# Optimization experiments

Hardware: AMD Instinct MI355X
Metric: run time of the kernel (lower is better)

The kernel has to match this reference:

```python
import jax, jax.numpy as jnp
import numpy as np


def setup_inputs() -> dict:
    key = jax.random.key(0)
    k1, k2, k3 = jax.random.split(key, 3)
    B, F, D = 8192, 4096, 1024
    x = jax.random.normal(k1, (B, D), dtype=jnp.float32)
    mu = jax.random.normal(k2, (F, D), dtype=jnp.float32)
    # keep scales strictly positive and well-conditioned
    scale_diag = jax.random.uniform(k3, (F, D), dtype=jnp.float32, minval=0.5, maxval=1.5)
    return {"x": x, "mu": mu, "scale_diag": scale_diag}


def reference(x, mu, scale_diag):
    # Unnormalized diag-Gaussian log prob for every (batch, feature) pair:
    #   out[b, f] = sum_d -0.5 * ((x[b,d] - mu[f,d]) / scale[f,d])^2
    # Expanded to GEMM form (quadratic expansion):
    #   -0.5 * ( x^2 @ inv2.T  -  2 * x @ (mu*inv2).T  +  sum_d mu^2*inv2 )
    inv2 = 1.0 / (scale_diag * scale_diag)            # [F, D]
    xx = jnp.matmul(x * x, inv2.T)                    # [B, F]
    xm = jnp.matmul(x, (mu * inv2).T)                 # [B, F]
    mm = jnp.sum(mu * mu * inv2, axis=-1)             # [F]
    return -0.5 * (xx - 2.0 * xm + mm[None, :])       # [B, F]
```

## Files before the change

### kernel.cpp

```cpp
#include <hip/hip_runtime.h>
#include <hip/hip_bf16.h>
#include <cstdint>

#define B_SZ 8192
#define F_SZ 4096
#define D_SZ 1024
#define K_SZ 2048

typedef __bf16 bf16x8 __attribute__((ext_vector_type(8)));
typedef float f32x4 __attribute__((ext_vector_type(4)));
typedef float fvec4 __attribute__((ext_vector_type(4)));
typedef unsigned short u16x4 __attribute__((ext_vector_type(4)));

__device__ __forceinline__ unsigned short f2bf(float f) {
    union { float f; unsigned u; } c; c.f = f;
    unsigned r = c.u + 0x7fff + ((c.u >> 16) & 1);
    return (unsigned short)(r >> 16);
}

__device__ __forceinline__ void async16(const void* g, void* l) {
    __builtin_amdgcn_global_load_lds(
        (__attribute__((address_space(1))) void*)g,
        (__attribute__((address_space(3))) void*)l, 16, 0, 0);
}

__global__ __launch_bounds__(256) void prep(const float* __restrict__ x,
                                            const float* __restrict__ mu,
                                            const float* __restrict__ sd,
                                            unsigned short* __restrict__ A,
                                            unsigned short* __restrict__ W,
                                            float* __restrict__ nmm) {
    const int tid = threadIdx.x;
    if (blockIdx.x < 4096) {
        const size_t o0 = (size_t)blockIdx.x * 2048 + tid * 4;
        fvec4 v0 = *(const fvec4*)(x + o0);
        fvec4 v1 = *(const fvec4*)(x + o0 + 1024);
        #pragma unroll
        for (int h = 0; h < 2; ++h) {
            fvec4 v = h ? v1 : v0;
            size_t oo = o0 + h * 1024;
            size_t b = oo >> 10;
            int d = (int)(oo & 1023);
            u16x4 xx, xs;
            xx.x = f2bf(v.x * v.x); xx.y = f2bf(v.y * v.y);
            xx.z = f2bf(v.z * v.z); xx.w = f2bf(v.w * v.w);
            xs.x = f2bf(v.x); xs.y = f2bf(v.y);
            xs.z = f2bf(v.z); xs.w = f2bf(v.w);
            *(u16x4*)(A + b * K_SZ + d) = xx;
            *(u16x4*)(A + b * K_SZ + 1024 + d) = xs;
        }
    } else {
        const int f = blockIdx.x - 4096;
        const int d = tid * 4;
        size_t off = (size_t)f * D_SZ + d;
        fvec4 m = *(const fvec4*)(mu + off);
        fvec4 s = *(const fvec4*)(sd + off);
        float i0 = 1.0f / (s.x * s.x), i1 = 1.0f / (s.y * s.y);
        float i2 = 1.0f / (s.z * s.z), i3 = 1.0f / (s.w * s.w);
        u16x4 wi, wm;
        wi.x = f2bf(i0); wi.y = f2bf(i1); wi.z = f2bf(i2); wi.w = f2bf(i3);
        wm.x = f2bf(-2.0f * m.x * i0); wm.y = f2bf(-2.0f * m.y * i1);
        wm.z = f2bf(-2.0f * m.z * i2); wm.w = f2bf(-2.0f * m.w * i3);
        size_t wb = (size_t)f * K_SZ + d;
        *(u16x4*)(W + wb) = wi;
        *(u16x4*)(W + wb + 1024) = wm;
        float mm = m.x * m.x * i0 + m.y * m.y * i1 + m.z * m.z * i2 + m.w * m.w * i3;
        #pragma unroll
        for (int o = 32; o > 0; o >>= 1) mm += __shfl_down(mm, o, 64);
        __shared__ float red[4];
        if ((tid & 63) == 0) red[tid >> 6] = mm;
        __syncthreads();
        if (tid == 0) nmm[f] = -0.5f * (red[0] + red[1] + red[2] + red[3]);
    }
}

__global__ __launch_bounds__(256) void gemm_bt(const unsigned short* __restrict__ A,
                                               const unsigned short* __restrict__ W,
                                               const float* __restrict__ nmm,
                                               float* __restrict__ out) {
    __shared__ __align__(16) unsigned short sA[128 * 32];
    __shared__ __align__(16) unsigned short sB[128 * 32];

    const int tid  = threadIdx.x;
    const int wave = tid >> 6;
    const int lane = tid & 63;
    const int wm = (wave >> 1) * 64;
    const int wn = (wave & 1) * 64;
    const int tileM = blockIdx.y * 128;
    const int tileN = blockIdx.x * 128;
    const int r16  = lane & 15;
    const int quad = lane >> 4;

    const int row0 = tid >> 2;
    const int col0 = (tid & 3) * 8;
    unsigned short* ldsA0 = sA + (wave * 64) * 8;
    unsigned short* ldsA1 = sA + (256 + wave * 64) * 8;
    unsigned short* ldsB0 = sB + (wave * 64) * 8;
    unsigned short* ldsB1 = sB + (256 + wave * 64) * 8;

    const f32x4 vzero = {0.f, 0.f, 0.f, 0.f};
    f32x4 acc[4][4];
    #pragma unroll
    for (int i = 0; i < 4; ++i)
        #pragma unroll
        for (int j = 0; j < 4; ++j) acc[i][j] = vzero;

    for (int k0 = 0; k0 < K_SZ; k0 += 32) {
        async16(A + (size_t)(tileM + row0) * K_SZ + k0 + col0, ldsA0);
        async16(A + (size_t)(tileM + row0 + 64) * K_SZ + k0 + col0, ldsA1);
        async16(W + (size_t)(tileN + row0) * K_SZ + k0 + col0, ldsB0);
        async16(W + (size_t)(tileN + row0 + 64) * K_SZ + k0 + col0, ldsB1);
        __syncthreads();

        bf16x8 af[4], bfr[4];
        #pragma unroll
        for (int i = 0; i < 4; ++i)
            af[i] = *(const bf16x8*)(sA + (wm + i * 16 + r16) * 32 + quad * 8);
        #pragma unroll
        for (int j = 0; j < 4; ++j)
            bfr[j] = *(const bf16x8*)(sB + (wn + j * 16 + r16) * 32 + quad * 8);
        #pragma unroll
        for (int i = 0; i < 4; ++i)
            #pragma unroll
            for (int j = 0; j < 4; ++j)
                acc[i][j] = __builtin_amdgcn_mfma_f32_16x16x32_bf16(
                    af[i], bfr[j], acc[i][j], 0, 0, 0);
        __syncthreads();
    }

    int   fc[4];
    float cj[4];
    #pragma unroll
    for (int j = 0; j < 4; ++j) {
        fc[j] = tileN + wn + j * 16 + r16;
        cj[j] = nmm[fc[j]];
    }
    #pragma unroll
    for (int i = 0; i < 4; ++i) {
        int mbase = tileM + wm + i * 16 + quad * 4;
        #pragma unroll
        for (int r = 0; r < 4; ++r) {
            float* orow = out + (size_t)(mbase + r) * F_SZ;
            #pragma unroll
            for (int j = 0; j < 4; ++j)
                orow[fc[j]] = -0.5f * acc[i][j][r] + cj[j];
        }
    }
}

extern "C" void kernel_launch(void* const* d_in, const int* in_sizes, int n_in,
                              void* d_out, int out_size, void* d_ws, size_t ws_size,
                              hipStream_t stream) {
    const float* x  = (const float*)d_in[0];
    const float* mu = (const float*)d_in[1];
    const float* sd = (const float*)d_in[2];
    float* out = (float*)d_out;

    unsigned short* A = (unsigned short*)d_ws;
    unsigned short* W = A + (size_t)B_SZ * K_SZ;
    float* nmm = (float*)(W + (size_t)F_SZ * K_SZ);

    prep<<<8192, 256, 0, stream>>>(x, mu, sd, A, W, nmm);
    gemm_bt<<<dim3(F_SZ / 128, B_SZ / 128), 256, 0, stream>>>(A, W, nmm, out);
}
```

Baseline: 332.2 us.

## Rewrite GEMM as 256x256 tile, 8-wave, double-buffered pipeline with swizzled LDS

The bf16 GEMM moves from 128x128 tiles with 4 waves and a single LDS buffer to 256x256 tiles with 8 waves. It double-buffers K=64 slabs and issues async global-to-LDS loads for the next stage between phases, using explicit vmcnt and lgkmcnt waits, raw barriers and setprio around the MFMA blocks. An XOR swizzle on LDS columns is meant to avoid bank conflicts. The goal is to hide global load latency behind MFMA work and raise arithmetic intensity per tile. The cost is 128KB of LDS, higher register pressure, and hand-tuned wait counts that may be fragile.

```diff
diff --git a/kernel.cpp b/kernel.cpp
--- a/kernel.cpp
+++ b/kernel.cpp
@@ -74,70 +74,123 @@
     }
 }
 
-__global__ __launch_bounds__(256) void gemm_bt(const unsigned short* __restrict__ A,
-                                               const unsigned short* __restrict__ W,
-                                               const float* __restrict__ nmm,
-                                               float* __restrict__ out) {
-    __shared__ __align__(16) unsigned short sA[128 * 32];
-    __shared__ __align__(16) unsigned short sB[128 * 32];
+__global__ __launch_bounds__(512, 2) void gemm_bt(const unsigned short* __restrict__ A,
+                                                  const unsigned short* __restrict__ W,
+                                                  const float* __restrict__ nmm,
+                                                  float* __restrict__ out) {
+    __shared__ __align__(16) unsigned short sA[2][2][256 * 32];
+    __shared__ __align__(16) unsigned short sB[2][2][256 * 32];
 
     const int tid  = threadIdx.x;
     const int wave = tid >> 6;
     const int lane = tid & 63;
-    const int wm = (wave >> 1) * 64;
-    const int wn = (wave & 1) * 64;
-    const int tileM = blockIdx.y * 128;
-    const int tileN = blockIdx.x * 128;
     const int r16  = lane & 15;
     const int quad = lane >> 4;
-
-    const int row0 = tid >> 2;
-    const int col0 = (tid & 3) * 8;
-    unsigned short* ldsA0 = sA + (wave * 64) * 8;
-    unsigned short* ldsA1 = sA + (256 + wave * 64) * 8;
-    unsigned short* ldsB0 = sB + (wave * 64) * 8;
-    unsigned short* ldsB1 = sB + (256 + wave * 64) * 8;
+    const int wmB  = (wave >> 2) * 128;
+    const int wnB  = (wave & 3) * 64;
+    const int tileM = blockIdx.y * 256;
+    const int tileN = blockIdx.x * 256;
+
+    const int srow   = tid >> 2;
+    const int schunk = tid & 3;
 
     const f32x4 vzero = {0.f, 0.f, 0.f, 0.f};
-    f32x4 acc[4][4];
+    f32x4 acc[8][4];
     #pragma unroll
-    for (int i = 0; i < 4; ++i)
+    for (int i = 0; i < 8; ++i)
         #pragma unroll
         for (int j = 0; j < 4; ++j) acc[i][j] = vzero;
 
-    for (int k0 = 0; k0 < K_SZ; k0 += 32) {
-        async16(A + (size_t)(tileM + row0) * K_SZ + k0 + col0, ldsA0);
-        async16(A + (size_t)(tileM + row0 + 64) * K_SZ + k0 + col0, ldsA1);
-        async16(W + (size_t)(tileN + row0) * K_SZ + k0 + col0, ldsB0);
-        async16(W + (size_t)(tileN + row0 + 64) * K_SZ + k0 + col0, ldsB1);
-        __syncthreads();
-
-        bf16x8 af[4], bfr[4];
-        #pragma unroll
-        for (int i = 0; i < 4; ++i)
-            af[i] = *(const bf16x8*)(sA + (wm + i * 16 + r16) * 32 + quad * 8);
-        #pragma unroll
-        for (int j = 0; j < 4; ++j)
-            bfr[j] = *(const bf16x8*)(sB + (wn + j * 16 + r16) * 32 + quad * 8);
-        #pragma unroll
-        for (int i = 0; i < 4; ++i)
-            #pragma unroll
-            for (int j = 0; j < 4; ++j)
-                acc[i][j] = __builtin_amdgcn_mfma_f32_16x16x32_bf16(
-                    af[i], bfr[j], acc[i][j], 0, 0, 0);
-        __syncthreads();
-    }
+    bf16x8 af[4], bfr[4];
+
+#define BARW() __builtin_amdgcn_s_barrier()
+#define LGK()  asm volatile("s_waitcnt lgkmcnt(0)" ::: "memory")
+#define VM4()  asm volatile("s_waitcnt vmcnt(4)" ::: "memory")
+#define VM0()  asm volatile("s_waitcnt vmcnt(0)" ::: "memory")
+
+#define STAGE(S, G, TB, DB, KK, KT)                                          \
+    { _Pragma("unroll")                                                      \
+      for (int is_ = 0; is_ < 2; ++is_) {                                    \
+          int rr_ = is_ * 128 + srow;                                        \
+          int gc_ = ((schunk ^ (rr_ & 3)) << 3);                             \
+          async16(G + (size_t)((TB) + rr_) * K_SZ + (KT) * 64 + (KK) * 32 + gc_, \
+                  &S[DB][KK][0] + is_ * 4096 + wave * 512);                  \
+      } }
+
+#define READ_A(I0, DB, KK)                                                   \
+    { _Pragma("unroll")                                                      \
+      for (int i_ = 0; i_ < 4; ++i_) {                                       \
+          int row_ = wmB + ((I0) + i_) * 16 + r16;                           \
+          af[i_] = *(const bf16x8*)(&sA[DB][KK][0] + row_ * 32 +             \
+                                    (((quad ^ row_) & 3) << 3));             \
+      } }
+
+#define READ_B(DB, KK)                                                       \
+    { _Pragma("unroll")                                                      \
+      for (int j_ = 0; j_ < 4; ++j_) {                                       \
+          int row_ = wnB + j_ * 16 + r16;                                    \
+          bfr[j_] = *(const bf16x8*)(&sB[DB][KK][0] + row_ * 32 +            \
+                                     (((quad ^ row_) & 3) << 3));            \
+      } }
+
+#define MFMA16(I0)                                                           \
+    __builtin_amdgcn_s_setprio(1);                                          \
+    { _Pragma("unroll")                                                      \
+      for (int i_ = 0; i_ < 4; ++i_)                                         \
+          _Pragma("unroll")                                                  \
+          for (int j_ = 0; j_ < 4; ++j_)                                     \
+              acc[(I0) + i_][j_] = __builtin_amdgcn_mfma_f32_16x16x32_bf16(  \
+                  af[i_], bfr[j_], acc[(I0) + i_][j_], 0, 0, 0); }           \
+    __builtin_amdgcn_s_setprio(0);
+
+#define PH(RB, I0, DB, KK, DOSTG, SBUF, G, TB, SDB, SKK, SKT, VM)            \
+    { if (RB) READ_B(DB, KK)                                                 \
+      READ_A(I0, DB, KK)                                                     \
+      if (DOSTG) STAGE(SBUF, G, TB, SDB, SKK, SKT)                           \
+      BARW(); LGK();                                                         \
+      MFMA16(I0)                                                             \
+      if ((VM) == 4) VM4(); else if ((VM) == 0) VM0();                       \
+      BARW(); }
+
+#define ITER(T, S58)                                                         \
+    PH(1, 0, 0, 0, 1,      sA, A, tileM, 1, 0, (T) + 1, -1)                  \
+    PH(0, 4, 0, 0, 1,      sB, W, tileN, 1, 0, (T) + 1, 4)                   \
+    PH(1, 0, 0, 1, 1,      sA, A, tileM, 1, 1, (T) + 1, -1)                  \
+    PH(0, 4, 0, 1, 1,      sB, W, tileN, 1, 1, (T) + 1, 4)                   \
+    PH(1, 0, 1, 0, (S58),  sA, A, tileM, 0, 0, (T) + 2, -1)                  \
+    PH(0, 4, 1, 0, (S58),  sB, W, tileN, 0, 0, (T) + 2, (S58) ? 4 : 0)       \
+    PH(1, 0, 1, 1, (S58),  sA, A, tileM, 0, 1, (T) + 2, -1)                  \
+    PH(0, 4, 1, 1, (S58),  sB, W, tileN, 0, 1, (T) + 2, -1)
+
+    STAGE(sA, A, tileM, 0, 0, 0)
+    STAGE(sB, W, tileN, 0, 0, 0)
+    STAGE(sA, A, tileM, 0, 1, 0)
+    STAGE(sB, W, tileN, 0, 1, 0)
+    VM4(); BARW();
+
+    #pragma unroll 1
+    for (int X = 0; X < 15; ++X) {
+        const int T = 2 * X;
+        ITER(T, 1)
+    }
+    {
+        const int T = 30;
+        ITER(T, 0)
+    }
+
+#undef PH
+#undef ITER
 
     int   fc[4];
     float cj[4];
     #pragma unroll
     for (int j = 0; j < 4; ++j) {
-        fc[j] = tileN + wn + j * 16 + r16;
+        fc[j] = tileN + wnB + j * 16 + r16;
         cj[j] = nmm[fc[j]];
     }
     #pragma unroll
-    for (int i = 0; i < 4; ++i) {
-        int mbase = tileM + wm + i * 16 + quad * 4;
+    for (int i = 0; i < 8; ++i) {
+        int mbase = tileM + wmB + i * 16 + quad * 4;
         #pragma unroll
         for (int r = 0; r < 4; ++r) {
             float* orow = out + (size_t)(mbase + r) * F_SZ;
@@ -161,5 +214,5 @@
     float* nmm = (float*)(W + (size_t)F_SZ * K_SZ);
 
     prep<<<8192, 256, 0, stream>>>(x, mu, sd, A, W, nmm);
-    gemm_bt<<<dim3(F_SZ / 128, B_SZ / 128), 256, 0, stream>>>(A, W, nmm, out);
-}
+    gemm_bt<<<dim3(F_SZ / 256, B_SZ / 256), 512, 0, stream>>>(A, W, nmm, out);
+}
```

New measurement: 316.7 us. -4.7%, faster.
